# Kernel tuning notes

Measured on AMD Instinct MI355X. Metric: run time of the kernel, lower is better.

The kernel has to match this reference:

```python
import jax, jax.numpy as jnp
import numpy as np

TOP_K = 2  # num_active_experts

def setup_inputs() -> dict:
    key = jax.random.key(0)
    ks = jax.random.split(key, 5)
    B, S = 4, 2048
    n1, n2, m1, m2, E = 32, 32, 64, 64, 8
    x = jax.random.normal(ks[0], (B, S, n1 * n2), dtype=jnp.float32)
    # gate weight (zero-init in the module; random here for nontrivial routing)
    Wg = jax.random.normal(ks[1], (E, n1 * n2), dtype=jnp.float32) * 0.02
    # BTT cores: W1 (n2, n1, m1, r), W2 (r, m1, n2, m2); r == num_experts
    W1 = jax.random.normal(ks[2], (n2, n1, m1, E), dtype=jnp.float32) / np.sqrt(n1).astype(np.float32)
    W2 = jax.random.normal(ks[3], (E, m1, n2, m2), dtype=jnp.float32) / np.sqrt(n2 * E).astype(np.float32)
    b = jax.random.normal(ks[4], (m1 * m2,), dtype=jnp.float32) * 0.01
    return {"x": x, "Wg": Wg, "W1": W1, "W2": W2, "b": b}

def reference(x, Wg, W1, W2, b):
    batch_shape = x.shape[:-1]
    xf = x.reshape(-1, x.shape[-1])          # (N, n1*n2)
    N = xf.shape[0]
    # gate: top-k + softmax over selected logits (softmax in fp32, as in torch)
    logits = xf @ Wg.T                        # (N, E)
    top_w, top_i = jax.lax.top_k(logits, TOP_K)
    top_w = jax.nn.softmax(top_w.astype(jnp.float32), axis=-1).astype(x.dtype) + 1e-6
    # scatter top-k weights into dense sparse_weights (N, E); inactive experts stay 0
    sparse_w = jnp.zeros_like(logits).at[jnp.arange(N)[:, None], top_i].set(top_w)
    # block-TT matmul with expert-weighted rank dimension
    n2, n1, m1, E = W1.shape
    xb = xf.reshape(N, n1, n2)
    z = jnp.einsum('bij,jikr->bjkr', xb, W1)          # (N, n2, m1, r): contract n1 per n2-block
    z = z * sparse_w[:, None, None, :]                # per-token expert/rank weighting
    y = jnp.einsum('bjkr,rkjl->bkl', z, W2)           # (N, m1, m2): contract n2, r per m1-block
    out = y.reshape(N, m1 * W2.shape[-1]) + b
    return out.reshape(*batch_shape, -1)
```

## Files before the change

### kernel.cpp

```cpp
#include <hip/hip_runtime.h>
#include <stdint.h>

#define NTOK 8192
#define DIM  1024
#define NE   8
#define NPAIR 28
#define OUTD 4096
#define MAXT16 539

typedef __attribute__((ext_vector_type(8))) short bf16x8;
typedef __attribute__((ext_vector_type(4))) float f32x4;

static __device__ __forceinline__ unsigned short f2bf(float f) {
    uint32_t u = __float_as_uint(f);
    u += 0x7fffu + ((u >> 16) & 1u);
    return (unsigned short)(u >> 16);
}

static __device__ __forceinline__ void barrier_lds() {
    asm volatile("s_waitcnt lgkmcnt(0)\n\ts_barrier" ::: "memory");
}

__global__ __launch_bounds__(256) void k_prep(const float* __restrict__ x,
                                              const float* __restrict__ Wg,
                                              const float* __restrict__ W1,
                                              const float* __restrict__ W2,
                                              unsigned short* __restrict__ w1m,
                                              unsigned short* __restrict__ w2m,
                                              int* __restrict__ pidTok,
                                              float* __restrict__ wgt) {
    __shared__ float smemf[8448];
    int bid = blockIdx.x;
    int tid = threadIdx.x;

    if (bid < 32) {
        int j = bid;
        unsigned short* lds = (unsigned short*)smemf;
        const float* src = W1 + (size_t)j * 16384;
        int f0 = tid * 64;
        #pragma unroll
        for (int c = 0; c < 16; ++c) {
            int f = f0 + c * 4;
            float4 v = *(const float4*)&src[f];
            int i = f >> 9, rem = f & 511;
            unsigned short* d = lds + i * 514 + rem;
            d[0] = f2bf(v.x); d[1] = f2bf(v.y); d[2] = f2bf(v.z); d[3] = f2bf(v.w);
        }
        __syncthreads();
        int e = tid >> 5, kp = tid & 31;
        #pragma unroll
        for (int dk = 0; dk < 2; ++dk) {
            int k = kp * 2 + dk;
            uint32_t q[16];
            #pragma unroll
            for (int c = 0; c < 16; ++c) {
                uint32_t lo = lds[(2 * c) * 514 + k * 8 + e];
                uint32_t hi = lds[(2 * c + 1) * 514 + k * 8 + e];
                q[c] = lo | (hi << 16);
            }
            unsigned short* dst = w1m + (((size_t)e * 32 + j) * 64 + k) * 32;
            #pragma unroll
            for (int c = 0; c < 4; ++c) {
                uint4 u; u.x = q[c*4]; u.y = q[c*4+1]; u.z = q[c*4+2]; u.w = q[c*4+3];
                *(uint4*)(dst + c * 8) = u;
            }
        }
    } else if (bid < 160) {
        int ek4 = bid - 32;
        unsigned short* lds = (unsigned short*)smemf;
        int sub = tid >> 6, l6 = tid & 63;
        const float* s2 = W2 + (size_t)ek4 * 8192 + sub * 2048 + l6 * 32;
        #pragma unroll
        for (int c = 0; c < 32; c += 4) {
            float4 v = *(const float4*)&s2[c];
            int f = l6 * 32 + c;
            int j = f >> 6, l = f & 63;
            unsigned short* d = lds + sub * 2112 + j * 66 + l;
            d[0] = f2bf(v.x); d[1] = f2bf(v.y); d[2] = f2bf(v.z); d[3] = f2bf(v.w);
        }
        __syncthreads();
        uint32_t q[16];
        #pragma unroll
        for (int c = 0; c < 16; ++c) {
            uint32_t lo = lds[sub * 2112 + (2 * c) * 66 + l6];
            uint32_t hi = lds[sub * 2112 + (2 * c + 1) * 66 + l6];
            q[c] = lo | (hi << 16);
        }
        unsigned short* dst = w2m + ((size_t)ek4 * 4 + sub) * 2048 + l6 * 32;
        #pragma unroll
        for (int c = 0; c < 4; ++c) {
            uint4 u; u.x = q[c*4]; u.y = q[c*4+1]; u.z = q[c*4+2]; u.w = q[c*4+3];
            *(uint4*)(dst + c * 8) = u;
        }
    } else {
        float* sWg = smemf;
        #pragma unroll
        for (int u = 0; u < 8; ++u) {
            int idx = u * 1024 + tid * 4;
            *(float4*)&sWg[idx] = *(const float4*)&Wg[idx];
        }
        __syncthreads();
        int w = tid >> 6, lane = tid & 63;
        int tokBase = (bid - 160) * 32 + w * 8;
        for (int it = 0; it < 8; ++it) {
            int tok = tokBase + it;
            float acc[NE];
            #pragma unroll
            for (int e = 0; e < NE; ++e) acc[e] = 0.f;
            const float* xr = x + (size_t)tok * DIM;
            #pragma unroll
            for (int c = 0; c < 4; ++c) {
                float4 xv = *(const float4*)&xr[c * 256 + lane * 4];
                #pragma unroll
                for (int e = 0; e < NE; ++e) {
                    float4 wv = *(const float4*)&sWg[e * 1024 + c * 256 + lane * 4];
                    acc[e] += xv.x * wv.x + xv.y * wv.y + xv.z * wv.z + xv.w * wv.w;
                }
            }
            #pragma unroll
            for (int e = 0; e < NE; ++e)
                #pragma unroll
                for (int off = 32; off > 0; off >>= 1)
                    acc[e] += __shfl_xor(acc[e], off, 64);
            if (lane == 0) {
                int i1 = 0; float v1 = acc[0];
                for (int e = 1; e < NE; ++e) if (acc[e] > v1) { v1 = acc[e]; i1 = e; }
                int i2 = -1; float v2 = -3.4e38f;
                for (int e = 0; e < NE; ++e) { if (e == i1) continue; if (acc[e] > v2) { v2 = acc[e]; i2 = e; } }
                float ex = expf(v2 - v1);
                float s  = 1.f / (1.f + ex);
                float w1v = s + 1e-6f;
                float w2v = ex * s + 1e-6f;
                int ea = min(i1, i2), eb = max(i1, i2);
                float wa = (i1 < i2) ? w1v : w2v;
                float wb = (i1 < i2) ? w2v : w1v;
                wgt[tok * 2 + 0] = wa;
                wgt[tok * 2 + 1] = wb;
                pidTok[tok] = ea * 7 - (ea * (ea - 1)) / 2 + (eb - ea - 1);
            }
        }
    }
}

__global__ __launch_bounds__(1024) void k_slots(const int* __restrict__ pidTok,
                                                int* __restrict__ tokmap,
                                                int4* __restrict__ tileDesc) {
    __shared__ int hist[NPAIR], base[NPAIR], cur[NPAIR];
    int tid = threadIdx.x;
    if (tid < NPAIR) { hist[tid] = 0; cur[tid] = 0; }
    __syncthreads();
    for (int i = tid; i < NTOK; i += 1024) atomicAdd(&hist[pidTok[i]], 1);
    __syncthreads();
    if (tid == 0) {
        int off = 0;
        for (int p = 0; p < NPAIR; ++p) { base[p] = off; off += hist[p]; }
    }
    __syncthreads();
    for (int i = tid; i < NTOK; i += 1024) {
        int p = pidTok[i];
        int pos = atomicAdd(&cur[p], 1);
        tokmap[base[p] + pos] = i;
    }
    __syncthreads();
    for (int s = tid; s < MAXT16; s += 1024) {
        int4 d; d.x = -1; d.y = 0; d.z = 0; d.w = 0;
        int toff = 0, soff = 0;
        for (int q = 0; q < NPAIR; ++q) {
            int c = hist[q];
            int nt = (c + 15) >> 4;
            if (d.x < 0 && s < toff + nt) {
                int lt = s - toff;
                d.x = q;
                d.y = soff + lt * 16;
                d.z = min(16, c - lt * 16);
            }
            toff += nt; soff += c;
        }
        tileDesc[s] = d;
    }
}

__global__ __launch_bounds__(256) void k_xg3(const float* __restrict__ x,
                                             const int* __restrict__ tokmap,
                                             unsigned short* __restrict__ xg3) {
    __shared__ float tile[8][1056];
    int s0 = blockIdx.x * 8;
    int tid = threadIdx.x;
    int r = tid >> 5, c = tid & 31;
    int tok = tokmap[s0 + r];
    const float* xr = x + (size_t)tok * DIM;
    #pragma unroll
    for (int u = 0; u < 8; ++u) {
        int d = u * 128 + c * 4;
        float4 v = *(const float4*)&xr[d];
        int d2 = d + (d >> 5);
        tile[r][d2 + 0] = v.x; tile[r][d2 + 1] = v.y;
        tile[r][d2 + 2] = v.z; tile[r][d2 + 3] = v.w;
    }
    __syncthreads();
    int sl = tid >> 5, j = tid & 31;
    float v[32];
    #pragma unroll
    for (int i = 0; i < 32; ++i) v[i] = tile[sl][i * 33 + j];
    unsigned short* orow = xg3 + ((size_t)j * NTOK + s0 + sl) * 32;
    #pragma unroll
    for (int ic = 0; ic < 4; ++ic) {
        uint4 pk;
        pk.x = (uint32_t)f2bf(v[ic * 8 + 0]) | ((uint32_t)f2bf(v[ic * 8 + 1]) << 16);
        pk.y = (uint32_t)f2bf(v[ic * 8 + 2]) | ((uint32_t)f2bf(v[ic * 8 + 3]) << 16);
        pk.z = (uint32_t)f2bf(v[ic * 8 + 4]) | ((uint32_t)f2bf(v[ic * 8 + 5]) << 16);
        pk.w = (uint32_t)f2bf(v[ic * 8 + 6]) | ((uint32_t)f2bf(v[ic * 8 + 7]) << 16);
        *(uint4*)(orow + ic * 8) = pk;
    }
}

__global__ __launch_bounds__(256, 3) void k_fz(const unsigned short* __restrict__ w1m,
                                               const unsigned short* __restrict__ w2m,
                                               const unsigned short* __restrict__ xg3,
                                               const float* __restrict__ bias,
                                               const int* __restrict__ tokmap,
                                               const float* __restrict__ wgt,
                                               const int4* __restrict__ tileDesc,
                                               float* __restrict__ out) {
    __shared__ unsigned short zls[8][2][4][16][8];
    __shared__ float ybuf[8192];

    int bid = blockIdx.x;
    int4 td = tileDesc[bid >> 2];
    int kb0 = (bid & 3) * 2;
    int p = td.x, s0 = td.y, cnt = td.z;
    if (p < 0) return;

    int a0 = 0, r0 = p;
    while (r0 >= 7 - a0) { r0 -= 7 - a0; ++a0; }
    int ea = a0, eb = a0 + 1 + r0;

    int tid = threadIdx.x;
    int w = tid >> 6, l = tid & 63;
    int lr = l & 15, lg = l >> 4;
    int e_lane = lr >> 3, kk = lr & 7;
    int my_e = e_lane ? eb : ea;

    float gs[4];
    #pragma unroll
    for (int r = 0; r < 4; ++r) {
        int tok = tokmap[min(s0 + lg * 4 + r, NTOK - 1)];
        float2 wv = *(const float2*)&wgt[tok * 2];
        gs[r] = e_lane ? wv.y : wv.x;
    }
    int tok4[4];
    #pragma unroll
    for (int tt = 0; tt < 4; ++tt)
        tok4[tt] = tokmap[min(s0 + w * 4 + tt, NTOK - 1)];

    bf16x8 a[8];
    int srow = min(s0 + lr, NTOK - 1);
    #pragma unroll
    for (int jj = 0; jj < 8; ++jj) {
        int j = w * 8 + jj;
        a[jj] = *(const bf16x8*)(xg3 + ((size_t)j * NTOK + srow) * 32 + lg * 8);
    }

    const f32x4 zero4 = {0.f, 0.f, 0.f, 0.f};
    const unsigned short* w1base = w1m + (((size_t)(my_e * 32 + w * 8) * 64) + kk) * 32 + lg * 8;

    bf16x8 w1f[8];
    #pragma unroll
    for (int jj = 0; jj < 8; ++jj)
        w1f[jj] = *(const bf16x8*)(w1base + (size_t)jj * 2048 + (size_t)kb0 * 256);

    auto phase1 = [&](int n) {
        f32x4 dj[8];
        #pragma unroll
        for (int jj = 0; jj < 8; ++jj)
            dj[jj] = __builtin_amdgcn_mfma_f32_16x16x32_bf16(a[jj], w1f[jj], zero4, 0, 0, 0);
        if (n + 1 < 2) {
            #pragma unroll
            for (int jj = 0; jj < 8; ++jj)
                w1f[jj] = *(const bf16x8*)(w1base + (size_t)jj * 2048 + (size_t)(kb0 + n + 1) * 256);
        }
        #pragma unroll
        for (int r = 0; r < 4; ++r) {
            float g = gs[r];
            int ts = (lg * 4 + r) ^ kk;
            uint4 pk;
            pk.x = (uint32_t)f2bf(dj[0][r] * g) | ((uint32_t)f2bf(dj[1][r] * g) << 16);
            pk.y = (uint32_t)f2bf(dj[2][r] * g) | ((uint32_t)f2bf(dj[3][r] * g) << 16);
            pk.z = (uint32_t)f2bf(dj[4][r] * g) | ((uint32_t)f2bf(dj[5][r] * g) << 16);
            pk.w = (uint32_t)f2bf(dj[6][r] * g) | ((uint32_t)f2bf(dj[7][r] * g) << 16);
            *(uint4*)&zls[kk][e_lane][w][ts][0] = pk;
        }
    };

    phase1(0);
    barrier_lds();

    for (int kbl = 0; kbl < 2; ++kbl) {
        int kb = kb0 + kbl;

        #pragma unroll
        for (int k = 0; k < 8; ++k) {
            int kg = kb * 8 + k;
            bf16x8 az0 = *(const bf16x8*)&zls[k][0][lg][lr ^ k][0];
            bf16x8 az1 = *(const bf16x8*)&zls[k][1][lg][lr ^ k][0];
            bf16x8 b0 = *(const bf16x8*)(w2m + (((size_t)ea * 64 + kg) * 64 + w * 16 + lr) * 32 + lg * 8);
            bf16x8 b1 = *(const bf16x8*)(w2m + (((size_t)eb * 64 + kg) * 64 + w * 16 + lr) * 32 + lg * 8);
            f32x4 acc = __builtin_amdgcn_mfma_f32_16x16x32_bf16(b0, az0, zero4, 0, 0, 0);
            acc = __builtin_amdgcn_mfma_f32_16x16x32_bf16(b1, az1, acc, 0, 0, 0);
            int pq = (k * 16 + w * 4 + lg) ^ (k & 1) ^ (lr & 7);
            *(f32x4*)&ybuf[lr * 512 + pq * 4] = acc;
        }
        barrier_lds();

        if (kbl < 1) phase1(kbl + 1);

        {
            f32x4 bv0 = *(const f32x4*)&bias[kb * 512 + l * 8];
            f32x4 bv1 = *(const f32x4*)&bias[kb * 512 + l * 8 + 4];
            int kq = l >> 3;
            int rbase = kq * 16 + (l & 7) * 2;
            #pragma unroll
            for (int tt = 0; tt < 4; ++tt) {
                int t = w * 4 + tt;
                if (t < cnt) {
                    int c = (kq & 1) ^ (t & 7);
                    f32x4 y0 = *(const f32x4*)&ybuf[t * 512 + ((rbase) ^ c) * 4];
                    f32x4 y1 = *(const f32x4*)&ybuf[t * 512 + ((rbase + 1) ^ c) * 4];
                    f32x4 o0 = y0 + bv0;
                    f32x4 o1 = y1 + bv1;
                    float* dst = out + (size_t)tok4[tt] * OUTD + kb * 512 + l * 8;
                    *(f32x4*)dst = o0;
                    *(f32x4*)(dst + 4) = o1;
                }
            }
        }
        if (kbl < 1) barrier_lds();
    }
}

extern "C" void kernel_launch(void* const* d_in, const int* in_sizes, int n_in,
                              void* d_out, int out_size, void* d_ws, size_t ws_size,
                              hipStream_t stream) {
    const float* x  = (const float*)d_in[0];
    const float* Wg = (const float*)d_in[1];
    const float* W1 = (const float*)d_in[2];
    const float* W2 = (const float*)d_in[3];
    const float* b  = (const float*)d_in[4];
    float* out = (float*)d_out;

    unsigned short* w1m = (unsigned short*)d_ws;
    unsigned short* w2m = w1m + 524288;
    unsigned short* xg3 = w2m + 1048576;
    int*   tokmap   = (int*)(xg3 + 8388608);
    float* wgt      = (float*)(tokmap + NTOK);
    int4*  tileDesc = (int4*)(wgt + 2 * NTOK);
    int*   pidTok   = (int*)(tileDesc + MAXT16);

    k_prep <<<416,  256, 0, stream>>>(x, Wg, W1, W2, w1m, w2m, pidTok, wgt);
    k_slots<<<1,   1024, 0, stream>>>(pidTok, tokmap, tileDesc);
    k_xg3  <<<1024, 256, 0, stream>>>(x, tokmap, xg3);
    k_fz   <<<MAXT16 * 4, 256, 0, stream>>>(w1m, w2m, xg3, b, tokmap, wgt, tileDesc, out);
}
```

Before: 98.29 us.

## Fuse token gather and bf16 conversion into main MoE-BTT kernel

Removes the separate k_xg3 pass that gathered routed tokens and wrote a bf16 transposed copy of x to workspace. Each k_fz block now loads its 16 tokens' fp32 rows directly, converts them to bf16 and stages them in the reused ybuf shared memory before forming MFMA operands. Block indexing is also remapped so the four quarter-blocks of a tile are spread across groups of eight, with a grid padded to a multiple of 32. This saves one launch and a full write and read of the gathered buffer, but each tile's x rows are now read and converted four times, once per quarter.

```diff
diff --git a/kernel.cpp b/kernel.cpp
--- a/kernel.cpp
+++ b/kernel.cpp
@@ -180,43 +180,9 @@
     }
 }
 
-__global__ __launch_bounds__(256) void k_xg3(const float* __restrict__ x,
-                                             const int* __restrict__ tokmap,
-                                             unsigned short* __restrict__ xg3) {
-    __shared__ float tile[8][1056];
-    int s0 = blockIdx.x * 8;
-    int tid = threadIdx.x;
-    int r = tid >> 5, c = tid & 31;
-    int tok = tokmap[s0 + r];
-    const float* xr = x + (size_t)tok * DIM;
-    #pragma unroll
-    for (int u = 0; u < 8; ++u) {
-        int d = u * 128 + c * 4;
-        float4 v = *(const float4*)&xr[d];
-        int d2 = d + (d >> 5);
-        tile[r][d2 + 0] = v.x; tile[r][d2 + 1] = v.y;
-        tile[r][d2 + 2] = v.z; tile[r][d2 + 3] = v.w;
-    }
-    __syncthreads();
-    int sl = tid >> 5, j = tid & 31;
-    float v[32];
-    #pragma unroll
-    for (int i = 0; i < 32; ++i) v[i] = tile[sl][i * 33 + j];
-    unsigned short* orow = xg3 + ((size_t)j * NTOK + s0 + sl) * 32;
-    #pragma unroll
-    for (int ic = 0; ic < 4; ++ic) {
-        uint4 pk;
-        pk.x = (uint32_t)f2bf(v[ic * 8 + 0]) | ((uint32_t)f2bf(v[ic * 8 + 1]) << 16);
-        pk.y = (uint32_t)f2bf(v[ic * 8 + 2]) | ((uint32_t)f2bf(v[ic * 8 + 3]) << 16);
-        pk.z = (uint32_t)f2bf(v[ic * 8 + 4]) | ((uint32_t)f2bf(v[ic * 8 + 5]) << 16);
-        pk.w = (uint32_t)f2bf(v[ic * 8 + 6]) | ((uint32_t)f2bf(v[ic * 8 + 7]) << 16);
-        *(uint4*)(orow + ic * 8) = pk;
-    }
-}
-
-__global__ __launch_bounds__(256, 3) void k_fz(const unsigned short* __restrict__ w1m,
+__global__ __launch_bounds__(256, 3) void k_fz(const float* __restrict__ x,
+                                               const unsigned short* __restrict__ w1m,
                                                const unsigned short* __restrict__ w2m,
-                                               const unsigned short* __restrict__ xg3,
                                                const float* __restrict__ bias,
                                                const int* __restrict__ tokmap,
                                                const float* __restrict__ wgt,
@@ -224,10 +190,14 @@
                                                float* __restrict__ out) {
     __shared__ unsigned short zls[8][2][4][16][8];
     __shared__ float ybuf[8192];
+    uint32_t* xs = (uint32_t*)ybuf;
 
     int bid = blockIdx.x;
-    int4 td = tileDesc[bid >> 2];
-    int kb0 = (bid & 3) * 2;
+    int tile = ((bid >> 5) << 3) | (bid & 7);
+    int quarter = (bid >> 3) & 3;
+    if (tile >= MAXT16) return;
+    int4 td = tileDesc[tile];
+    int kb0 = quarter * 2;
     int p = td.x, s0 = td.y, cnt = td.z;
     if (p < 0) return;
 
@@ -253,14 +223,6 @@
     for (int tt = 0; tt < 4; ++tt)
         tok4[tt] = tokmap[min(s0 + w * 4 + tt, NTOK - 1)];
 
-    bf16x8 a[8];
-    int srow = min(s0 + lr, NTOK - 1);
-    #pragma unroll
-    for (int jj = 0; jj < 8; ++jj) {
-        int j = w * 8 + jj;
-        a[jj] = *(const bf16x8*)(xg3 + ((size_t)j * NTOK + srow) * 32 + lg * 8);
-    }
-
     const f32x4 zero4 = {0.f, 0.f, 0.f, 0.f};
     const unsigned short* w1base = w1m + (((size_t)(my_e * 32 + w * 8) * 64) + kk) * 32 + lg * 8;
 
@@ -268,6 +230,30 @@
     #pragma unroll
     for (int jj = 0; jj < 8; ++jj)
         w1f[jj] = *(const bf16x8*)(w1base + (size_t)jj * 2048 + (size_t)kb0 * 256);
+
+    {
+        int t = tid >> 4, q = tid & 15;
+        int tok = tokmap[min(s0 + t, NTOK - 1)];
+        const float* xr = x + (size_t)tok * DIM + q * 64;
+        float4 va[16];
+        #pragma unroll
+        for (int c = 0; c < 16; ++c) va[c] = *(const float4*)&xr[c * 4];
+        uint32_t* xrow = xs + t * 16 + q;
+        #pragma unroll
+        for (int j = 0; j < 32; ++j) {
+            float lo = ((const float*)&va[j >> 2])[j & 3];
+            float hi = ((const float*)&va[8 + (j >> 2)])[j & 3];
+            xrow[j * 256] = (uint32_t)f2bf(lo) | ((uint32_t)f2bf(hi) << 16);
+        }
+    }
+    barrier_lds();
+
+    bf16x8 a[8];
+    #pragma unroll
+    for (int jj = 0; jj < 8; ++jj) {
+        int j = w * 8 + jj;
+        a[jj] = *(const bf16x8*)(xs + j * 256 + lr * 16 + lg * 4);
+    }
 
     auto phase1 = [&](int n) {
         f32x4 dj[8];
@@ -350,14 +336,12 @@
 
     unsigned short* w1m = (unsigned short*)d_ws;
     unsigned short* w2m = w1m + 524288;
-    unsigned short* xg3 = w2m + 1048576;
-    int*   tokmap   = (int*)(xg3 + 8388608);
+    int*   tokmap   = (int*)(w2m + 1048576);
     float* wgt      = (float*)(tokmap + NTOK);
     int4*  tileDesc = (int4*)(wgt + 2 * NTOK);
     int*   pidTok   = (int*)(tileDesc + MAXT16);
 
     k_prep <<<416,  256, 0, stream>>>(x, Wg, W1, W2, w1m, w2m, pidTok, wgt);
     k_slots<<<1,   1024, 0, stream>>>(pidTok, tokmap, tileDesc);
-    k_xg3  <<<1024, 256, 0, stream>>>(x, tokmap, xg3);
-    k_fz   <<<MAXT16 * 4, 256, 0, stream>>>(w1m, w2m, xg3, b, tokmap, wgt, tileDesc, out);
-}
+    k_fz   <<<2176, 256, 0, stream>>>(x, w1m, w2m, b, tokmap, wgt, tileDesc, out);
+}
```

Measured after the change: 94.28 us. -4.1%, faster.
